# Performance work log

Measured on AMD Instinct MI355X. Metric: run time of the kernel, lower is better.

The kernel has to match this reference:

```python
import jax, jax.numpy as jnp
import numpy as np

T = 32400   # bs*H*W BEV queries (1*180*180)
S = 16896   # bs*num_cams*h*w image keys (1*6*32*88)
E = 256     # embed_dim
H = 8       # num_heads
D = 32      # head_dim
MAXL = 32   # max interval length (ref_num_f)


def _mlp(x, w1, b1, w2, b2):
    # nn.Sequential(Linear(E,2E), ReLU, Linear(2E,E))
    return jax.nn.relu(x @ w1 + b1) @ w2 + b2


def setup_inputs() -> dict:
    k0 = jax.random.key(0)
    ks = jax.random.split(k0, 8)
    # ragged interval structure: every BEV cell has an interval of length (idx%32)+1
    lengths = (np.arange(T) % MAXL) + 1
    starts = np.concatenate([np.zeros(1, np.int64), np.cumsum(lengths)[:-1]])
    N = int(lengths.sum())  # 534472 frustum points
    ranks_bev = np.repeat(np.arange(T), lengths)          # sorted by BEV cell
    rng = np.random.default_rng(0)
    ranks_feat = rng.integers(0, S, size=N)               # which key/value row each point reads

    def lin(k, fi, fo):
        return jax.random.normal(k, (fi, fo), jnp.float32) * (1.0 / np.sqrt(fi))

    key_feat = jax.random.normal(ks[1], (S, E), jnp.float32)
    return dict(
        query_depth=jax.random.normal(ks[0], (T, E), jnp.float32),
        key=key_feat,
        value=key_feat,  # module asserts torch.equal(key, value)
        q_w1=lin(ks[2], E, 2 * E), q_b1=jnp.zeros((2 * E,), jnp.float32),
        q_w2=lin(ks[3], 2 * E, E), q_b2=jnp.zeros((E,), jnp.float32),
        k_w1=lin(ks[4], E, 2 * E), k_b1=jnp.zeros((2 * E,), jnp.float32),
        k_w2=lin(ks[5], 2 * E, E), k_b2=jnp.zeros((E,), jnp.float32),
        ranks_feat_f=jnp.asarray(ranks_feat, jnp.int32),
        ranks_bev_f=jnp.asarray(ranks_bev, jnp.int32),
        interval_starts_f=jnp.asarray(starts, jnp.int32),
        interval_lengths_f=jnp.asarray(lengths, jnp.int32),
        ref_num=MAXL,
    )


def reference(query_depth, key, value,
              q_w1, q_b1, q_w2, q_b2,
              k_w1, k_b1, k_w2, k_b2,
              ranks_feat_f, ranks_bev_f,
              interval_starts_f, interval_lengths_f, ref_num):
    scaling = 1.0 / jnp.sqrt(jnp.float32(D))
    q = (_mlp(query_depth, q_w1, q_b1, q_w2, q_b2) * scaling).reshape(T, H, D)
    k = _mlp(key, k_w1, k_b1, k_w2, k_b2).reshape(S, H, D)
    v = value.reshape(S, H, D)

    N = ranks_bev_f.shape[0]
    pt = jnp.arange(N, dtype=jnp.int32)
    # interval id of each point (intervals are contiguous, sorted by start)
    iid = jnp.searchsorted(interval_starts_f, pt, side='right') - 1
    ranks_ref = pt - interval_starts_f[iid]  # within-interval slot, in [0, ref_num)

    # per-point raw attention logit: q[bev] . k[feat] per head  -> [N, H]
    w = jnp.einsum('nhd,nhd->nh', q[ranks_bev_f], k[ranks_feat_f])

    # scatter into ragged weight tensor [T, H, ref_num]; padding masked to -1e9
    attn = jnp.full((T, H, ref_num), -1e9, jnp.float32)
    attn = attn.at[ranks_bev_f, :, ranks_ref].set(w)
    attn = jax.nn.softmax(attn, axis=-1)

    # gather normalized weights back per point and scatter-combine values
    wp = attn[ranks_bev_f, :, ranks_ref]          # [N, H]
    vp = v[ranks_feat_f]                          # [N, H, D]
    out = jnp.zeros((T, H, D), jnp.float32).at[ranks_bev_f].add(wp[:, :, None] * vp)
    return out.reshape(T, E)
```

## Files before the change

kernel.cpp:

```cpp
#include <hip/hip_runtime.h>
#include <hip/hip_bf16.h>
#include <cstdint>
#include <cstddef>

constexpr int T_Q   = 32400;
constexpr int T_PAD = 32512;
constexpr int S_K   = 16896;
constexpr int E_DIM = 256;
constexpr int HID   = 512;

typedef __bf16 bf16x8 __attribute__((ext_vector_type(8)));
typedef float  f32x4  __attribute__((ext_vector_type(4)));
typedef unsigned short ushort8v __attribute__((ext_vector_type(8)));

__device__ __forceinline__ void async16(const __hip_bfloat16* gp, __hip_bfloat16* lp) {
    __builtin_amdgcn_global_load_lds(
        (const __attribute__((address_space(1))) void*)(gp),
        (__attribute__((address_space(3))) void*)(lp), 16, 0, 0);
}

__device__ __forceinline__ float b2f(unsigned short u) {
    return __uint_as_float(((unsigned)u) << 16);
}

constexpr int NB_K = (S_K * E_DIM / 4) / 256;
constexpr int NB_PREP = NB_K + 128;

__global__ __launch_bounds__(256) void prep(
    const float* __restrict__ val_in,
    const float* __restrict__ s0, const float* __restrict__ s1,
    const float* __restrict__ s2, const float* __restrict__ s3,
    __hip_bfloat16* __restrict__ kvB,
    __hip_bfloat16* __restrict__ d0, __hip_bfloat16* __restrict__ d1,
    __hip_bfloat16* __restrict__ d2, __hip_bfloat16* __restrict__ d3) {
    __shared__ float tb[64][65];
    const int b = blockIdx.x;
    const int tid = threadIdx.x;

    if (b < NB_K) {
        int i = (b * 256 + tid) * 4;
        float4 f = *(const float4*)(val_in + i);
        union { ushort4 u4; __hip_bfloat16 bb[4]; } cv;
        cv.bb[0] = __float2bfloat16(f.x);
        cv.bb[1] = __float2bfloat16(f.y);
        cv.bb[2] = __float2bfloat16(f.z);
        cv.bb[3] = __float2bfloat16(f.w);
        int r = i >> 8, c = i & 255;
        *(ushort4*)(kvB + (size_t)r * 512 + 256 + c) = cv.u4;
        return;
    }

    int tloc = b - NB_K;
    int m = tloc >> 5;
    int tt = tloc & 31;
    const float* S = m == 0 ? s0 : m == 1 ? s1 : m == 2 ? s2 : s3;
    __hip_bfloat16* D = m == 0 ? d0 : m == 1 ? d1 : m == 2 ? d2 : d3;
    int Kd, Nd, kt, nt;
    if ((m & 1) == 0) { Kd = 256; Nd = 512; kt = tt & 3; nt = tt >> 2; }
    else              { Kd = 512; Nd = 256; kt = tt & 7; nt = tt >> 3; }
    int tx = tid & 63, ty = tid >> 6;
#pragma unroll
    for (int p = 0; p < 16; ++p) {
        int row = ty * 16 + p;
        tb[row][tx] = S[(size_t)(kt * 64 + row) * Nd + nt * 64 + tx];
    }
    __syncthreads();
#pragma unroll
    for (int p = 0; p < 16; ++p) {
        int row = ty * 16 + p;
        D[(size_t)(nt * 64 + row) * Kd + kt * 64 + tx] = __float2bfloat16(tb[tx][row]);
    }
}


constexpr int MLP_QT = T_PAD / 64;
constexpr int MLP_KT = S_K / 64;
constexpr int MLP_NB = MLP_QT + MLP_KT;

__global__ __launch_bounds__(512, 4) void mlp_fused(
    const float* __restrict__ Aq, const float* __restrict__ Ak,
    const __hip_bfloat16* __restrict__ W1q, const __hip_bfloat16* __restrict__ W1k,
    const __hip_bfloat16* __restrict__ W2q, const __hip_bfloat16* __restrict__ W2k,
    const float* __restrict__ b1q, const float* __restrict__ b1k,
    const float* __restrict__ b2q, const float* __restrict__ b2k,
    __hip_bfloat16* __restrict__ Cq, __hip_bfloat16* __restrict__ Ck,
    float scaleq, int qtiles) {
    __shared__ __align__(16) __hip_bfloat16 Aslab[64 * 64];
    __shared__ __align__(16) __hip_bfloat16 Bs[256 * 64];
    __shared__ __align__(16) __hip_bfloat16 Hs[64 * 256];

    const int b = blockIdx.x;
    const bool isq = b < qtiles;
    const float* A  = isq ? Aq : Ak;
    const __hip_bfloat16* W1 = isq ? W1q : W1k;
    const __hip_bfloat16* W2 = isq ? W2q : W2k;
    const float* b1 = isq ? b1q : b1k;
    const float* b2 = isq ? b2q : b2k;
    __hip_bfloat16* C = isq ? Cq : Ck;
    const int ldc = isq ? E_DIM : 512;
    const float scale = isq ? scaleq : 1.0f;
    const int mrow0 = (isq ? b : b - qtiles) * 64;
    const int rowlim = isq ? T_Q : S_K;

    const int tid = threadIdx.x;
    const int w = tid >> 6, l = tid & 63;
    const int lm = l & 15, lq = l >> 4;
    const int wm = w >> 2;
    const int wn4 = w & 3;
    const int srow8 = l >> 3;
    const int u8 = l & 7;
    const int pu8 = u8 ^ srow8;
    const int scolB = (u8 ^ srow8) << 3;

    f32x4 acc2[2][4] = {};

#pragma unroll 1
    for (int nh = 0; nh < 2; ++nh) {
        f32x4 acc[2][4] = {};
#pragma unroll 1
        for (int st = 0; st < 4; ++st) {
            const int k0 = st * 64;
            {
                int r = w * 8 + srow8;
                int gr = mrow0 + r;
                float4 f0 = make_float4(0.f, 0.f, 0.f, 0.f);
                float4 f1 = make_float4(0.f, 0.f, 0.f, 0.f);
                if (gr < rowlim) {
                    const float* ap = A + (size_t)gr * 256 + k0 + u8 * 8;
                    f0 = *(const float4*)ap;
                    f1 = *(const float4*)(ap + 4);
                }
                union { bf16x8 v; __hip_bfloat16 bb[8]; } cv;
                cv.bb[0] = __float2bfloat16(f0.x); cv.bb[1] = __float2bfloat16(f0.y);
                cv.bb[2] = __float2bfloat16(f0.z); cv.bb[3] = __float2bfloat16(f0.w);
                cv.bb[4] = __float2bfloat16(f1.x); cv.bb[5] = __float2bfloat16(f1.y);
                cv.bb[6] = __float2bfloat16(f1.z); cv.bb[7] = __float2bfloat16(f1.w);
                *(bf16x8*)(Aslab + r * 64 + pu8 * 8) = cv.v;
            }
#pragma unroll
            for (int c = 0; c < 4; ++c) {
                int r = w * 32 + c * 8 + srow8;
                async16(W1 + (size_t)(nh * 256 + r) * 256 + k0 + scolB,
                        Bs + (w * 32 + c * 8) * 64);
            }
            __syncthreads();
#pragma unroll
            for (int ks = 0; ks < 2; ++ks) {
                bf16x8 af[2], bfr[4];
#pragma unroll
                for (int mi = 0; mi < 2; ++mi) {
                    int row = wm * 32 + mi * 16 + lm;
                    int pu = (ks * 4 + lq) ^ (row & 7);
                    af[mi] = *(const bf16x8*)(Aslab + row * 64 + pu * 8);
                }
#pragma unroll
                for (int ni = 0; ni < 4; ++ni) {
                    int brow = wn4 * 64 + ni * 16 + lm;
                    int pu = (ks * 4 + lq) ^ (brow & 7);
                    bfr[ni] = *(const bf16x8*)(Bs + brow * 64 + pu * 8);
                }
#pragma unroll
                for (int mi = 0; mi < 2; ++mi)
#pragma unroll
                    for (int ni = 0; ni < 4; ++ni)
                        acc[mi][ni] = __builtin_amdgcn_mfma_f32_16x16x32_bf16(
                            af[mi], bfr[ni], acc[mi][ni], 0, 0, 0);
            }
            __syncthreads();
        }

#pragma unroll
        for (int ni = 0; ni < 4; ++ni) {
            int col = wn4 * 64 + ni * 16 + lm;
            float bv = b1[nh * 256 + col];
            int un = col >> 3, el = col & 7;
#pragma unroll
            for (int mi = 0; mi < 2; ++mi) {
#pragma unroll
                for (int r = 0; r < 4; ++r) {
                    int row = wm * 32 + mi * 16 + lq * 4 + r;
                    float vv = fmaxf(acc[mi][ni][r] + bv, 0.f);
                    int pu = (un & 24) | ((un & 7) ^ (row & 7));
                    Hs[row * 256 + pu * 8 + el] = __float2bfloat16(vv);
                }
            }
        }

#pragma unroll 1
        for (int st = 0; st < 4; ++st) {
            const int k0 = st * 64;
#pragma unroll
            for (int c = 0; c < 4; ++c) {
                int r = w * 32 + c * 8 + srow8;
                async16(W2 + (size_t)r * 512 + nh * 256 + k0 + scolB,
                        Bs + (w * 32 + c * 8) * 64);
            }
            __syncthreads();
#pragma unroll
            for (int ks = 0; ks < 2; ++ks) {
                bf16x8 af[2], bfr[4];
#pragma unroll
                for (int mi = 0; mi < 2; ++mi) {
                    int row = wm * 32 + mi * 16 + lm;
                    int un = st * 8 + ks * 4 + lq;
                    int pu = (un & 24) | ((un & 7) ^ (row & 7));
                    af[mi] = *(const bf16x8*)(Hs + row * 256 + pu * 8);
                }
#pragma unroll
                for (int ni = 0; ni < 4; ++ni) {
                    int brow = wn4 * 64 + ni * 16 + lm;
                    int pu = (ks * 4 + lq) ^ (brow & 7);
                    bfr[ni] = *(const bf16x8*)(Bs + brow * 64 + pu * 8);
                }
#pragma unroll
                for (int mi = 0; mi < 2; ++mi)
#pragma unroll
                    for (int ni = 0; ni < 4; ++ni)
                        acc2[mi][ni] = __builtin_amdgcn_mfma_f32_16x16x32_bf16(
                            af[mi], bfr[ni], acc2[mi][ni], 0, 0, 0);
            }
            __syncthreads();
        }
    }

#pragma unroll
    for (int ni = 0; ni < 4; ++ni) {
        int col = wn4 * 64 + ni * 16 + lm;
        float bv = b2[col];
#pragma unroll
        for (int mi = 0; mi < 2; ++mi) {
            size_t rowb = (size_t)mrow0 + wm * 32 + mi * 16 + lq * 4;
#pragma unroll
            for (int r = 0; r < 4; ++r) {
                float vv = (acc2[mi][ni][r] + bv) * scale;
                C[(rowb + r) * ldc + col] = __float2bfloat16(vv);
            }
        }
    }
}


#define PREFP(KB, VB, C)                                                     \
    {                                                                        \
        int f_ = __shfl(myf, (C) + half);                                    \
        const __hip_bfloat16* p_ = kv + ((size_t)f_ << 9) + (sub << 3);      \
        KB = *(const ushort8v*)p_;                                           \
        VB = *(const ushort8v*)(p_ + 256);                                   \
    }

#define PROCP(KB, VB, C)                                                     \
    {                                                                        \
        float wv = 0.f;                                                      \
        _Pragma("unroll") for (int i = 0; i < 8; ++i)                        \
            wv = fmaf(qf[i], b2f(KB[i]), wv);                                \
        wv += __shfl_xor(wv, 1);                                             \
        wv += __shfl_xor(wv, 2);                                             \
        float sc = ((C) + half < L) ? wv : -1e30f;                           \
        float so = __shfl_xor(sc, 32);                                       \
        float pm = fmaxf(sc, so);                                            \
        if (__all(pm <= m)) {                                                \
            float p = __expf(sc - m);                                        \
            s += p;                                                          \
            _Pragma("unroll") for (int i = 0; i < 8; ++i)                    \
                a[i] = fmaf(p, b2f(VB[i]), a[i]);                            \
        } else {                                                             \
            float mn = fmaxf(m, pm);                                         \
            float al = __expf(m - mn);                                       \
            float p  = __expf(sc - mn);                                      \
            m = mn;                                                          \
            s = fmaf(s, al, p);                                              \
            _Pragma("unroll") for (int i = 0; i < 8; ++i)                    \
                a[i] = fmaf(p, b2f(VB[i]), a[i] * al);                       \
        }                                                                    \
    }

#define STEPP(KB, VB, J)                                                     \
    if (c + (J) < L) {                                                       \
        PROCP(KB, VB, c + (J));                                              \
        if (c + (J) + 8 < L) PREFP(KB, VB, c + (J) + 8);                     \
    }

constexpr int ATTN_BLOCKS = 2026;

__global__ __launch_bounds__(256) void attn_kernel(
    const __hip_bfloat16* __restrict__ q,
    const __hip_bfloat16* __restrict__ kv,
    const int* __restrict__ rf,
    const int* __restrict__ starts,
    const int* __restrict__ lens,
    float* __restrict__ out) {
    const int wid = threadIdx.x >> 6;
    const int l = threadIdx.x & 63;
    const int sub = l & 31, half = l >> 5;
    const int tstride = gridDim.x * 4;

    for (int t = blockIdx.x * 4 + wid; t < T_Q; t += tstride) {
        int su = __builtin_amdgcn_readfirstlane(starts[t]);
        int L  = __builtin_amdgcn_readfirstlane(lens[t]);

        int li = l < L - 1 ? l : L - 1;
        int myf = rf[su + li];

        ushort8v qu = *(const ushort8v*)(q + (size_t)t * 256 + sub * 8);
        float qf[8];
#pragma unroll
        for (int i = 0; i < 8; ++i) qf[i] = b2f(qu[i]);

        float m = -INFINITY, s = 0.f;
        float a[8] = {0.f, 0.f, 0.f, 0.f, 0.f, 0.f, 0.f, 0.f};

        ushort8v k0 = {}, v0 = {}, k1 = {}, v1 = {};
        ushort8v k2 = {}, v2 = {}, k3 = {}, v3 = {};
        PREFP(k0, v0, 0);
        if (L > 2) PREFP(k1, v1, 2);
        if (L > 4) PREFP(k2, v2, 4);
        if (L > 6) PREFP(k3, v3, 6);

        for (int c = 0; c < L; c += 8) {
            STEPP(k0, v0, 0)
            STEPP(k1, v1, 2)
            STEPP(k2, v2, 4)
            STEPP(k3, v3, 6)
        }

        float st = s + __shfl_xor(s, 32);
#pragma unroll
        for (int i = 0; i < 8; ++i) a[i] += __shfl_xor(a[i], 32);

        if (half) {
            float inv = 1.f / st;
            float* op = out + (size_t)t * 256 + sub * 8;
            float4 o0, o1;
            o0.x = a[0] * inv; o0.y = a[1] * inv; o0.z = a[2] * inv; o0.w = a[3] * inv;
            o1.x = a[4] * inv; o1.y = a[5] * inv; o1.z = a[6] * inv; o1.w = a[7] * inv;
            *(float4*)op = o0;
            *(float4*)(op + 4) = o1;
        }
    }
}

extern "C" void kernel_launch(void* const* d_in, const int* in_sizes, int n_in,
                              void* d_out, int out_size, void* d_ws, size_t ws_size,
                              hipStream_t stream) {
    const float* q_in   = (const float*)d_in[0];
    const float* key_in = (const float*)d_in[1];
    const float* val_in = (const float*)d_in[2];
    const float* q_w1   = (const float*)d_in[3];
    const float* q_b1   = (const float*)d_in[4];
    const float* q_w2   = (const float*)d_in[5];
    const float* q_b2   = (const float*)d_in[6];
    const float* k_w1   = (const float*)d_in[7];
    const float* k_b1   = (const float*)d_in[8];
    const float* k_w2   = (const float*)d_in[9];
    const float* k_b2   = (const float*)d_in[10];
    const int* ranks_feat = (const int*)d_in[11];
    const int* starts     = (const int*)d_in[13];
    const int* lens       = (const int*)d_in[14];
    float* out = (float*)d_out;

    char* ws = (char*)d_ws;
    size_t off = 0;
    auto alloc = [&](size_t bytes) {
        char* p = ws + off;
        off += (bytes + 255) & ~(size_t)255;
        return p;
    };
    __hip_bfloat16* qMl  = (__hip_bfloat16*)alloc((size_t)T_PAD * E_DIM * 2);
    __hip_bfloat16* kvB  = (__hip_bfloat16*)alloc((size_t)S_K * 512 * 2);
    __hip_bfloat16* w1qT = (__hip_bfloat16*)alloc((size_t)HID * E_DIM * 2);
    __hip_bfloat16* w2qT = (__hip_bfloat16*)alloc((size_t)E_DIM * HID * 2);
    __hip_bfloat16* w1kT = (__hip_bfloat16*)alloc((size_t)HID * E_DIM * 2);
    __hip_bfloat16* w2kT = (__hip_bfloat16*)alloc((size_t)E_DIM * HID * 2);
    (void)ws_size; (void)n_in; (void)out_size; (void)in_sizes;

    prep<<<NB_PREP, 256, 0, stream>>>(val_in, q_w1, q_w2, k_w1, k_w2,
                                      kvB, w1qT, w2qT, w1kT, w2kT);

    const float qscale = 0.17677669529663687f;

    mlp_fused<<<MLP_NB, 512, 0, stream>>>(
        q_in, key_in, w1qT, w1kT, w2qT, w2kT,
        q_b1, k_b1, q_b2, k_b2, qMl, kvB, qscale, MLP_QT);

    attn_kernel<<<ATTN_BLOCKS, 256, 0, stream>>>(qMl, kvB, ranks_feat, starts, lens, out);
}
```

Before: 273.4 us.

## Double MLP row tile to 128 and fold value bf16 conversion into MLP kernel

The fused MLP kernel now processes 128 rows per block instead of 64. Each warp computes 4x4 MFMA tiles, so every weight slab loaded into LDS is reused across twice as many rows, halving weight traffic per row. The value-to-bf16 conversion moves out of the prep kernel into the tail of the key-side MLP blocks, which shrinks prep to only the weight transposes. In exchange, LDS use and register pressure rise, occupancy drops (launch bounds go from 4 to 2 blocks per unit), and there are half as many blocks.

```diff
diff --git a/kernel.cpp b/kernel.cpp
--- a/kernel.cpp
+++ b/kernel.cpp
@@ -23,36 +23,17 @@
     return __uint_as_float(((unsigned)u) << 16);
 }
 
-constexpr int NB_K = (S_K * E_DIM / 4) / 256;
-constexpr int NB_PREP = NB_K + 128;
-
 __global__ __launch_bounds__(256) void prep(
-    const float* __restrict__ val_in,
     const float* __restrict__ s0, const float* __restrict__ s1,
     const float* __restrict__ s2, const float* __restrict__ s3,
-    __hip_bfloat16* __restrict__ kvB,
     __hip_bfloat16* __restrict__ d0, __hip_bfloat16* __restrict__ d1,
     __hip_bfloat16* __restrict__ d2, __hip_bfloat16* __restrict__ d3) {
     __shared__ float tb[64][65];
     const int b = blockIdx.x;
     const int tid = threadIdx.x;
 
-    if (b < NB_K) {
-        int i = (b * 256 + tid) * 4;
-        float4 f = *(const float4*)(val_in + i);
-        union { ushort4 u4; __hip_bfloat16 bb[4]; } cv;
-        cv.bb[0] = __float2bfloat16(f.x);
-        cv.bb[1] = __float2bfloat16(f.y);
-        cv.bb[2] = __float2bfloat16(f.z);
-        cv.bb[3] = __float2bfloat16(f.w);
-        int r = i >> 8, c = i & 255;
-        *(ushort4*)(kvB + (size_t)r * 512 + 256 + c) = cv.u4;
-        return;
-    }
-
-    int tloc = b - NB_K;
-    int m = tloc >> 5;
-    int tt = tloc & 31;
+    int m = b >> 5;
+    int tt = b & 31;
     const float* S = m == 0 ? s0 : m == 1 ? s1 : m == 2 ? s2 : s3;
     __hip_bfloat16* D = m == 0 ? d0 : m == 1 ? d1 : m == 2 ? d2 : d3;
     int Kd, Nd, kt, nt;
@@ -73,21 +54,22 @@
 }
 
 
-constexpr int MLP_QT = T_PAD / 64;
-constexpr int MLP_KT = S_K / 64;
+constexpr int MLP_QT = T_PAD / 128;
+constexpr int MLP_KT = S_K / 128;
 constexpr int MLP_NB = MLP_QT + MLP_KT;
 
-__global__ __launch_bounds__(512, 4) void mlp_fused(
+__global__ __launch_bounds__(512, 2) void mlp_fused(
     const float* __restrict__ Aq, const float* __restrict__ Ak,
+    const float* __restrict__ val_in,
     const __hip_bfloat16* __restrict__ W1q, const __hip_bfloat16* __restrict__ W1k,
     const __hip_bfloat16* __restrict__ W2q, const __hip_bfloat16* __restrict__ W2k,
     const float* __restrict__ b1q, const float* __restrict__ b1k,
     const float* __restrict__ b2q, const float* __restrict__ b2k,
     __hip_bfloat16* __restrict__ Cq, __hip_bfloat16* __restrict__ Ck,
     float scaleq, int qtiles) {
-    __shared__ __align__(16) __hip_bfloat16 Aslab[64 * 64];
+    __shared__ __align__(16) __hip_bfloat16 Aslab[128 * 64];
     __shared__ __align__(16) __hip_bfloat16 Bs[256 * 64];
-    __shared__ __align__(16) __hip_bfloat16 Hs[64 * 256];
+    __shared__ __align__(16) __hip_bfloat16 Hs[128 * 256];
 
     const int b = blockIdx.x;
     const bool isq = b < qtiles;
@@ -99,7 +81,7 @@
     __hip_bfloat16* C = isq ? Cq : Ck;
     const int ldc = isq ? E_DIM : 512;
     const float scale = isq ? scaleq : 1.0f;
-    const int mrow0 = (isq ? b : b - qtiles) * 64;
+    const int mrow0 = (isq ? b : b - qtiles) * 128;
     const int rowlim = isq ? T_Q : S_K;
 
     const int tid = threadIdx.x;
@@ -109,24 +91,26 @@
     const int wn4 = w & 3;
     const int srow8 = l >> 3;
     const int u8 = l & 7;
-    const int pu8 = u8 ^ srow8;
     const int scolB = (u8 ^ srow8) << 3;
 
-    f32x4 acc2[2][4] = {};
+    f32x4 acc2[4][4] = {};
 
 #pragma unroll 1
     for (int nh = 0; nh < 2; ++nh) {
-        f32x4 acc[2][4] = {};
+        f32x4 acc[4][4] = {};
 #pragma unroll 1
         for (int st = 0; st < 4; ++st) {
             const int k0 = st * 64;
-            {
-                int r = w * 8 + srow8;
+#pragma unroll
+            for (int c = 0; c < 2; ++c) {
+                int idx = tid + c * 512;
+                int r = idx >> 3;
+                int u = idx & 7;
                 int gr = mrow0 + r;
                 float4 f0 = make_float4(0.f, 0.f, 0.f, 0.f);
                 float4 f1 = make_float4(0.f, 0.f, 0.f, 0.f);
                 if (gr < rowlim) {
-                    const float* ap = A + (size_t)gr * 256 + k0 + u8 * 8;
+                    const float* ap = A + (size_t)gr * 256 + k0 + u * 8;
                     f0 = *(const float4*)ap;
                     f1 = *(const float4*)(ap + 4);
                 }
@@ -135,7 +119,8 @@
                 cv.bb[2] = __float2bfloat16(f0.z); cv.bb[3] = __float2bfloat16(f0.w);
                 cv.bb[4] = __float2bfloat16(f1.x); cv.bb[5] = __float2bfloat16(f1.y);
                 cv.bb[6] = __float2bfloat16(f1.z); cv.bb[7] = __float2bfloat16(f1.w);
-                *(bf16x8*)(Aslab + r * 64 + pu8 * 8) = cv.v;
+                int pu = u ^ (r & 7);
+                *(bf16x8*)(Aslab + r * 64 + pu * 8) = cv.v;
             }
 #pragma unroll
             for (int c = 0; c < 4; ++c) {
@@ -146,10 +131,10 @@
             __syncthreads();
 #pragma unroll
             for (int ks = 0; ks < 2; ++ks) {
-                bf16x8 af[2], bfr[4];
-#pragma unroll
-                for (int mi = 0; mi < 2; ++mi) {
-                    int row = wm * 32 + mi * 16 + lm;
+                bf16x8 af[4], bfr[4];
+#pragma unroll
+                for (int mi = 0; mi < 4; ++mi) {
+                    int row = wm * 64 + mi * 16 + lm;
                     int pu = (ks * 4 + lq) ^ (row & 7);
                     af[mi] = *(const bf16x8*)(Aslab + row * 64 + pu * 8);
                 }
@@ -160,7 +145,7 @@
                     bfr[ni] = *(const bf16x8*)(Bs + brow * 64 + pu * 8);
                 }
 #pragma unroll
-                for (int mi = 0; mi < 2; ++mi)
+                for (int mi = 0; mi < 4; ++mi)
 #pragma unroll
                     for (int ni = 0; ni < 4; ++ni)
                         acc[mi][ni] = __builtin_amdgcn_mfma_f32_16x16x32_bf16(
@@ -175,10 +160,10 @@
             float bv = b1[nh * 256 + col];
             int un = col >> 3, el = col & 7;
 #pragma unroll
-            for (int mi = 0; mi < 2; ++mi) {
+            for (int mi = 0; mi < 4; ++mi) {
 #pragma unroll
                 for (int r = 0; r < 4; ++r) {
-                    int row = wm * 32 + mi * 16 + lq * 4 + r;
+                    int row = wm * 64 + mi * 16 + lq * 4 + r;
                     float vv = fmaxf(acc[mi][ni][r] + bv, 0.f);
                     int pu = (un & 24) | ((un & 7) ^ (row & 7));
                     Hs[row * 256 + pu * 8 + el] = __float2bfloat16(vv);
@@ -198,10 +183,10 @@
             __syncthreads();
 #pragma unroll
             for (int ks = 0; ks < 2; ++ks) {
-                bf16x8 af[2], bfr[4];
-#pragma unroll
-                for (int mi = 0; mi < 2; ++mi) {
-                    int row = wm * 32 + mi * 16 + lm;
+                bf16x8 af[4], bfr[4];
+#pragma unroll
+                for (int mi = 0; mi < 4; ++mi) {
+                    int row = wm * 64 + mi * 16 + lm;
                     int un = st * 8 + ks * 4 + lq;
                     int pu = (un & 24) | ((un & 7) ^ (row & 7));
                     af[mi] = *(const bf16x8*)(Hs + row * 256 + pu * 8);
@@ -213,7 +198,7 @@
                     bfr[ni] = *(const bf16x8*)(Bs + brow * 64 + pu * 8);
                 }
 #pragma unroll
-                for (int mi = 0; mi < 2; ++mi)
+                for (int mi = 0; mi < 4; ++mi)
 #pragma unroll
                     for (int ni = 0; ni < 4; ++ni)
                         acc2[mi][ni] = __builtin_amdgcn_mfma_f32_16x16x32_bf16(
@@ -228,13 +213,30 @@
         int col = wn4 * 64 + ni * 16 + lm;
         float bv = b2[col];
 #pragma unroll
-        for (int mi = 0; mi < 2; ++mi) {
-            size_t rowb = (size_t)mrow0 + wm * 32 + mi * 16 + lq * 4;
+        for (int mi = 0; mi < 4; ++mi) {
+            size_t rowb = (size_t)mrow0 + wm * 64 + mi * 16 + lq * 4;
 #pragma unroll
             for (int r = 0; r < 4; ++r) {
                 float vv = (acc2[mi][ni][r] + bv) * scale;
                 C[(rowb + r) * ldc + col] = __float2bfloat16(vv);
             }
+        }
+    }
+
+    if (!isq) {
+#pragma unroll
+        for (int i = 0; i < 16; ++i) {
+            int idx = tid + i * 512;
+            int r = idx >> 6;
+            int c4 = idx & 63;
+            int gr = mrow0 + r;
+            float4 f = *(const float4*)(val_in + (size_t)gr * 256 + c4 * 4);
+            union { ushort4 u4; __hip_bfloat16 bb[4]; } cv;
+            cv.bb[0] = __float2bfloat16(f.x);
+            cv.bb[1] = __float2bfloat16(f.y);
+            cv.bb[2] = __float2bfloat16(f.z);
+            cv.bb[3] = __float2bfloat16(f.w);
+            *(ushort4*)(Ck + (size_t)gr * 512 + 256 + c4 * 4) = cv.u4;
         }
     }
 }
@@ -373,13 +375,13 @@
     __hip_bfloat16* w2kT = (__hip_bfloat16*)alloc((size_t)E_DIM * HID * 2);
     (void)ws_size; (void)n_in; (void)out_size; (void)in_sizes;
 
-    prep<<<NB_PREP, 256, 0, stream>>>(val_in, q_w1, q_w2, k_w1, k_w2,
-                                      kvB, w1qT, w2qT, w1kT, w2kT);
+    prep<<<128, 256, 0, stream>>>(q_w1, q_w2, k_w1, k_w2,
+                                  w1qT, w2qT, w1kT, w2kT);
 
     const float qscale = 0.17677669529663687f;
 
     mlp_fused<<<MLP_NB, 512, 0, stream>>>(
-        q_in, key_in, w1qT, w1kT, w2qT, w2kT,
+        q_in, key_in, val_in, w1qT, w1kT, w2qT, w2kT,
         q_b1, k_b1, q_b2, k_b2, qMl, kvB, qscale, MLP_QT);
 
     attn_kernel<<<ATTN_BLOCKS, 256, 0, stream>>>(qMl, kvB, ranks_feat, starts, lens, out);
```

Measured after the change: 264.7 us. -3.2%, faster.

## Pre-cast MLP inputs to bf16 and read GEMM operands directly from global memory

Applied to the files above, without the earlier changes.

The prep kernel now casts both query and key inputs to a combined bf16 buffer, and the value cast moves into the tail of the key MLP blocks. The fused MLP kernel drops its LDS staging for the A slab and the weight tiles and loads MFMA fragments straight from global memory (relying on L2 for weight reuse), removing most per-stage barriers and unrolling the k loops. This cuts LDS traffic and synchronisation, and frees LDS that may allow more resident blocks. In exchange it adds an extra round trip of the bf16 input buffer through memory and issues uncoalesced 16-byte global loads per lane.

```diff
diff --git a/kernel.cpp b/kernel.cpp
--- a/kernel.cpp
+++ b/kernel.cpp
@@ -13,44 +13,52 @@
 typedef float  f32x4  __attribute__((ext_vector_type(4)));
 typedef unsigned short ushort8v __attribute__((ext_vector_type(8)));
 
-__device__ __forceinline__ void async16(const __hip_bfloat16* gp, __hip_bfloat16* lp) {
-    __builtin_amdgcn_global_load_lds(
-        (const __attribute__((address_space(1))) void*)(gp),
-        (__attribute__((address_space(3))) void*)(lp), 16, 0, 0);
-}
-
 __device__ __forceinline__ float b2f(unsigned short u) {
     return __uint_as_float(((unsigned)u) << 16);
 }
 
-constexpr int NB_K = (S_K * E_DIM / 4) / 256;
-constexpr int NB_PREP = NB_K + 128;
+constexpr int AB_ROWS = T_PAD + S_K;
+constexpr int CAST_NB = AB_ROWS * 256 / 2048;
+constexpr int PREP_NB = CAST_NB + 128;
 
 __global__ __launch_bounds__(256) void prep(
-    const float* __restrict__ val_in,
+    const float* __restrict__ q_in, const float* __restrict__ key_in,
+    __hip_bfloat16* __restrict__ Abf,
     const float* __restrict__ s0, const float* __restrict__ s1,
     const float* __restrict__ s2, const float* __restrict__ s3,
-    __hip_bfloat16* __restrict__ kvB,
     __hip_bfloat16* __restrict__ d0, __hip_bfloat16* __restrict__ d1,
     __hip_bfloat16* __restrict__ d2, __hip_bfloat16* __restrict__ d3) {
     __shared__ float tb[64][65];
     const int b = blockIdx.x;
     const int tid = threadIdx.x;
 
-    if (b < NB_K) {
-        int i = (b * 256 + tid) * 4;
-        float4 f = *(const float4*)(val_in + i);
-        union { ushort4 u4; __hip_bfloat16 bb[4]; } cv;
-        cv.bb[0] = __float2bfloat16(f.x);
-        cv.bb[1] = __float2bfloat16(f.y);
-        cv.bb[2] = __float2bfloat16(f.z);
-        cv.bb[3] = __float2bfloat16(f.w);
-        int r = i >> 8, c = i & 255;
-        *(ushort4*)(kvB + (size_t)r * 512 + 256 + c) = cv.u4;
+    if (b < CAST_NB) {
+        size_t base = ((size_t)b * 256 + tid) * 8;
+        int row = (int)(base >> 8);
+        int c = (int)(base & 255);
+        float4 f0 = make_float4(0.f, 0.f, 0.f, 0.f);
+        float4 f1 = make_float4(0.f, 0.f, 0.f, 0.f);
+        if (row < T_PAD) {
+            if (row < T_Q) {
+                const float* p = q_in + (size_t)row * 256 + c;
+                f0 = *(const float4*)p;
+                f1 = *(const float4*)(p + 4);
+            }
+        } else {
+            const float* p = key_in + (size_t)(row - T_PAD) * 256 + c;
+            f0 = *(const float4*)p;
+            f1 = *(const float4*)(p + 4);
+        }
+        union { bf16x8 v; __hip_bfloat16 bb[8]; } cv;
+        cv.bb[0] = __float2bfloat16(f0.x); cv.bb[1] = __float2bfloat16(f0.y);
+        cv.bb[2] = __float2bfloat16(f0.z); cv.bb[3] = __float2bfloat16(f0.w);
+        cv.bb[4] = __float2bfloat16(f1.x); cv.bb[5] = __float2bfloat16(f1.y);
+        cv.bb[6] = __float2bfloat16(f1.z); cv.bb[7] = __float2bfloat16(f1.w);
+        *(bf16x8*)(Abf + (size_t)row * 256 + c) = cv.v;
         return;
     }
 
-    int tloc = b - NB_K;
+    int tloc = b - CAST_NB;
     int m = tloc >> 5;
     int tt = tloc & 31;
     const float* S = m == 0 ? s0 : m == 1 ? s1 : m == 2 ? s2 : s3;
@@ -78,20 +86,18 @@
 constexpr int MLP_NB = MLP_QT + MLP_KT;
 
 __global__ __launch_bounds__(512, 4) void mlp_fused(
-    const float* __restrict__ Aq, const float* __restrict__ Ak,
+    const __hip_bfloat16* __restrict__ Abf,
+    const float* __restrict__ val_in,
     const __hip_bfloat16* __restrict__ W1q, const __hip_bfloat16* __restrict__ W1k,
     const __hip_bfloat16* __restrict__ W2q, const __hip_bfloat16* __restrict__ W2k,
     const float* __restrict__ b1q, const float* __restrict__ b1k,
     const float* __restrict__ b2q, const float* __restrict__ b2k,
     __hip_bfloat16* __restrict__ Cq, __hip_bfloat16* __restrict__ Ck,
     float scaleq, int qtiles) {
-    __shared__ __align__(16) __hip_bfloat16 Aslab[64 * 64];
-    __shared__ __align__(16) __hip_bfloat16 Bs[256 * 64];
     __shared__ __align__(16) __hip_bfloat16 Hs[64 * 256];
 
     const int b = blockIdx.x;
     const bool isq = b < qtiles;
-    const float* A  = isq ? Aq : Ak;
     const __hip_bfloat16* W1 = isq ? W1q : W1k;
     const __hip_bfloat16* W2 = isq ? W2q : W2k;
     const float* b1 = isq ? b1q : b1k;
@@ -100,64 +106,38 @@
     const int ldc = isq ? E_DIM : 512;
     const float scale = isq ? scaleq : 1.0f;
     const int mrow0 = (isq ? b : b - qtiles) * 64;
-    const int rowlim = isq ? T_Q : S_K;
+    const size_t arow0 = (size_t)(isq ? b * 64 : T_PAD + (b - qtiles) * 64);
 
     const int tid = threadIdx.x;
     const int w = tid >> 6, l = tid & 63;
     const int lm = l & 15, lq = l >> 4;
     const int wm = w >> 2;
     const int wn4 = w & 3;
-    const int srow8 = l >> 3;
-    const int u8 = l & 7;
-    const int pu8 = u8 ^ srow8;
-    const int scolB = (u8 ^ srow8) << 3;
+
+    const __hip_bfloat16* Arow[2];
+#pragma unroll
+    for (int mi = 0; mi < 2; ++mi)
+        Arow[mi] = Abf + (arow0 + wm * 32 + mi * 16 + lm) * 256;
 
     f32x4 acc2[2][4] = {};
 
 #pragma unroll 1
     for (int nh = 0; nh < 2; ++nh) {
         f32x4 acc[2][4] = {};
-#pragma unroll 1
+#pragma unroll
         for (int st = 0; st < 4; ++st) {
             const int k0 = st * 64;
-            {
-                int r = w * 8 + srow8;
-                int gr = mrow0 + r;
-                float4 f0 = make_float4(0.f, 0.f, 0.f, 0.f);
-                float4 f1 = make_float4(0.f, 0.f, 0.f, 0.f);
-                if (gr < rowlim) {
-                    const float* ap = A + (size_t)gr * 256 + k0 + u8 * 8;
-                    f0 = *(const float4*)ap;
-                    f1 = *(const float4*)(ap + 4);
-                }
-                union { bf16x8 v; __hip_bfloat16 bb[8]; } cv;
-                cv.bb[0] = __float2bfloat16(f0.x); cv.bb[1] = __float2bfloat16(f0.y);
-                cv.bb[2] = __float2bfloat16(f0.z); cv.bb[3] = __float2bfloat16(f0.w);
-                cv.bb[4] = __float2bfloat16(f1.x); cv.bb[5] = __float2bfloat16(f1.y);
-                cv.bb[6] = __float2bfloat16(f1.z); cv.bb[7] = __float2bfloat16(f1.w);
-                *(bf16x8*)(Aslab + r * 64 + pu8 * 8) = cv.v;
-            }
-#pragma unroll
-            for (int c = 0; c < 4; ++c) {
-                int r = w * 32 + c * 8 + srow8;
-                async16(W1 + (size_t)(nh * 256 + r) * 256 + k0 + scolB,
-                        Bs + (w * 32 + c * 8) * 64);
-            }
-            __syncthreads();
 #pragma unroll
             for (int ks = 0; ks < 2; ++ks) {
+                const int kc = k0 + (ks * 4 + lq) * 8;
                 bf16x8 af[2], bfr[4];
 #pragma unroll
-                for (int mi = 0; mi < 2; ++mi) {
-                    int row = wm * 32 + mi * 16 + lm;
-                    int pu = (ks * 4 + lq) ^ (row & 7);
-                    af[mi] = *(const bf16x8*)(Aslab + row * 64 + pu * 8);
-                }
+                for (int mi = 0; mi < 2; ++mi)
+                    af[mi] = *(const bf16x8*)(Arow[mi] + kc);
 #pragma unroll
                 for (int ni = 0; ni < 4; ++ni) {
-                    int brow = wn4 * 64 + ni * 16 + lm;
-                    int pu = (ks * 4 + lq) ^ (brow & 7);
-                    bfr[ni] = *(const bf16x8*)(Bs + brow * 64 + pu * 8);
+                    int brow = nh * 256 + wn4 * 64 + ni * 16 + lm;
+                    bfr[ni] = *(const bf16x8*)(W1 + (size_t)brow * 256 + kc);
                 }
 #pragma unroll
                 for (int mi = 0; mi < 2; ++mi)
@@ -166,8 +146,9 @@
                         acc[mi][ni] = __builtin_amdgcn_mfma_f32_16x16x32_bf16(
                             af[mi], bfr[ni], acc[mi][ni], 0, 0, 0);
             }
-            __syncthreads();
-        }
+        }
+
+        __syncthreads();
 
 #pragma unroll
         for (int ni = 0; ni < 4; ++ni) {
@@ -185,17 +166,11 @@
                 }
             }
         }
-
-#pragma unroll 1
+        __syncthreads();
+
+#pragma unroll
         for (int st = 0; st < 4; ++st) {
             const int k0 = st * 64;
-#pragma unroll
-            for (int c = 0; c < 4; ++c) {
-                int r = w * 32 + c * 8 + srow8;
-                async16(W2 + (size_t)r * 512 + nh * 256 + k0 + scolB,
-                        Bs + (w * 32 + c * 8) * 64);
-            }
-            __syncthreads();
 #pragma unroll
             for (int ks = 0; ks < 2; ++ks) {
                 bf16x8 af[2], bfr[4];
@@ -209,8 +184,8 @@
 #pragma unroll
                 for (int ni = 0; ni < 4; ++ni) {
                     int brow = wn4 * 64 + ni * 16 + lm;
-                    int pu = (ks * 4 + lq) ^ (brow & 7);
-                    bfr[ni] = *(const bf16x8*)(Bs + brow * 64 + pu * 8);
+                    bfr[ni] = *(const bf16x8*)(
+                        W2 + (size_t)brow * 512 + nh * 256 + k0 + (ks * 4 + lq) * 8);
                 }
 #pragma unroll
                 for (int mi = 0; mi < 2; ++mi)
@@ -219,7 +194,6 @@
                         acc2[mi][ni] = __builtin_amdgcn_mfma_f32_16x16x32_bf16(
                             af[mi], bfr[ni], acc2[mi][ni], 0, 0, 0);
             }
-            __syncthreads();
         }
     }
 
@@ -235,6 +209,23 @@
                 float vv = (acc2[mi][ni][r] + bv) * scale;
                 C[(rowb + r) * ldc + col] = __float2bfloat16(vv);
             }
+        }
+    }
+
+    if (!isq) {
+#pragma unroll
+        for (int i = 0; i < 8; ++i) {
+            int idx = tid + i * 512;
+            int r = idx >> 6;
+            int c4 = idx & 63;
+            int gr = mrow0 + r;
+            float4 f = *(const float4*)(val_in + (size_t)gr * 256 + c4 * 4);
+            union { ushort4 u4; __hip_bfloat16 bb[4]; } cv;
+            cv.bb[0] = __float2bfloat16(f.x);
+            cv.bb[1] = __float2bfloat16(f.y);
+            cv.bb[2] = __float2bfloat16(f.z);
+            cv.bb[3] = __float2bfloat16(f.w);
+            *(ushort4*)(Ck + (size_t)gr * 512 + 256 + c4 * 4) = cv.u4;
         }
     }
 }
@@ -367,19 +358,21 @@
     };
     __hip_bfloat16* qMl  = (__hip_bfloat16*)alloc((size_t)T_PAD * E_DIM * 2);
     __hip_bfloat16* kvB  = (__hip_bfloat16*)alloc((size_t)S_K * 512 * 2);
+    __hip_bfloat16* Abf  = (__hip_bfloat16*)alloc((size_t)AB_ROWS * 256 * 2);
     __hip_bfloat16* w1qT = (__hip_bfloat16*)alloc((size_t)HID * E_DIM * 2);
     __hip_bfloat16* w2qT = (__hip_bfloat16*)alloc((size_t)E_DIM * HID * 2);
     __hip_bfloat16* w1kT = (__hip_bfloat16*)alloc((size_t)HID * E_DIM * 2);
     __hip_bfloat16* w2kT = (__hip_bfloat16*)alloc((size_t)E_DIM * HID * 2);
     (void)ws_size; (void)n_in; (void)out_size; (void)in_sizes;
 
-    prep<<<NB_PREP, 256, 0, stream>>>(val_in, q_w1, q_w2, k_w1, k_w2,
-                                      kvB, w1qT, w2qT, w1kT, w2kT);
+    prep<<<PREP_NB, 256, 0, stream>>>(q_in, key_in, Abf,
+                                      q_w1, q_w2, k_w1, k_w2,
+                                      w1qT, w2qT, w1kT, w2kT);
 
     const float qscale = 0.17677669529663687f;
 
     mlp_fused<<<MLP_NB, 512, 0, stream>>>(
-        q_in, key_in, w1qT, w1kT, w2qT, w2kT,
+        Abf, val_in, w1qT, w1kT, w2qT, w2kT,
         q_b1, k_b1, q_b2, k_b2, qMl, kvB, qscale, MLP_QT);
 
     attn_kernel<<<ATTN_BLOCKS, 256, 0, stream>>>(qMl, kvB, ranks_feat, starts, lens, out);
```

Result: slower. 398.4 us (+45.7%).

## Fuse value bf16 conversion into MLP kernel and deepen attention prefetch pipeline

Applied to the files above, without the earlier changes.

The fp32-to-bf16 conversion of the value rows, which used to run in the prep kernel, now happens inside the key-side MLP blocks. Each block writes the second half of the interleaved kv buffer for its own 64 rows, so prep only transposes the weights. Separately, the attention loop gets a fifth prefetch register pair, so five key/value pairs are in flight instead of four. The extra registers could lower occupancy in the attention kernel, and the MLP key blocks take on more memory traffic.

```diff
diff --git a/kernel.cpp b/kernel.cpp
--- a/kernel.cpp
+++ b/kernel.cpp
@@ -23,36 +23,17 @@
     return __uint_as_float(((unsigned)u) << 16);
 }
 
-constexpr int NB_K = (S_K * E_DIM / 4) / 256;
-constexpr int NB_PREP = NB_K + 128;
-
 __global__ __launch_bounds__(256) void prep(
-    const float* __restrict__ val_in,
     const float* __restrict__ s0, const float* __restrict__ s1,
     const float* __restrict__ s2, const float* __restrict__ s3,
-    __hip_bfloat16* __restrict__ kvB,
     __hip_bfloat16* __restrict__ d0, __hip_bfloat16* __restrict__ d1,
     __hip_bfloat16* __restrict__ d2, __hip_bfloat16* __restrict__ d3) {
     __shared__ float tb[64][65];
     const int b = blockIdx.x;
     const int tid = threadIdx.x;
 
-    if (b < NB_K) {
-        int i = (b * 256 + tid) * 4;
-        float4 f = *(const float4*)(val_in + i);
-        union { ushort4 u4; __hip_bfloat16 bb[4]; } cv;
-        cv.bb[0] = __float2bfloat16(f.x);
-        cv.bb[1] = __float2bfloat16(f.y);
-        cv.bb[2] = __float2bfloat16(f.z);
-        cv.bb[3] = __float2bfloat16(f.w);
-        int r = i >> 8, c = i & 255;
-        *(ushort4*)(kvB + (size_t)r * 512 + 256 + c) = cv.u4;
-        return;
-    }
-
-    int tloc = b - NB_K;
-    int m = tloc >> 5;
-    int tt = tloc & 31;
+    int m = b >> 5;
+    int tt = b & 31;
     const float* S = m == 0 ? s0 : m == 1 ? s1 : m == 2 ? s2 : s3;
     __hip_bfloat16* D = m == 0 ? d0 : m == 1 ? d1 : m == 2 ? d2 : d3;
     int Kd, Nd, kt, nt;
@@ -79,6 +60,7 @@
 
 __global__ __launch_bounds__(512, 4) void mlp_fused(
     const float* __restrict__ Aq, const float* __restrict__ Ak,
+    const float* __restrict__ val_in,
     const __hip_bfloat16* __restrict__ W1q, const __hip_bfloat16* __restrict__ W1k,
     const __hip_bfloat16* __restrict__ W2q, const __hip_bfloat16* __restrict__ W2k,
     const float* __restrict__ b1q, const float* __restrict__ b1k,
@@ -111,6 +93,23 @@
     const int u8 = l & 7;
     const int pu8 = u8 ^ srow8;
     const int scolB = (u8 ^ srow8) << 3;
+
+    if (!isq) {
+#pragma unroll
+        for (int i = 0; i < 8; ++i) {
+            int idx = tid + i * 512;
+            int r = idx >> 6;
+            int c4 = idx & 63;
+            int gr = mrow0 + r;
+            float4 f = *(const float4*)(val_in + (size_t)gr * 256 + c4 * 4);
+            union { ushort4 u4; __hip_bfloat16 bb[4]; } cv;
+            cv.bb[0] = __float2bfloat16(f.x);
+            cv.bb[1] = __float2bfloat16(f.y);
+            cv.bb[2] = __float2bfloat16(f.z);
+            cv.bb[3] = __float2bfloat16(f.w);
+            *(ushort4*)(Ck + (size_t)gr * 512 + 256 + c4 * 4) = cv.u4;
+        }
+    }
 
     f32x4 acc2[2][4] = {};
 
@@ -277,7 +276,7 @@
 #define STEPP(KB, VB, J)                                                     \
     if (c + (J) < L) {                                                       \
         PROCP(KB, VB, c + (J));                                              \
-        if (c + (J) + 8 < L) PREFP(KB, VB, c + (J) + 8);                     \
+        if (c + (J) + 10 < L) PREFP(KB, VB, c + (J) + 10);                   \
     }
 
 constexpr int ATTN_BLOCKS = 2026;
@@ -309,18 +308,20 @@
         float m = -INFINITY, s = 0.f;
         float a[8] = {0.f, 0.f, 0.f, 0.f, 0.f, 0.f, 0.f, 0.f};
 
-        ushort8v k0 = {}, v0 = {}, k1 = {}, v1 = {};
-        ushort8v k2 = {}, v2 = {}, k3 = {}, v3 = {};
+        ushort8v k0 = {}, v0 = {}, k1 = {}, v1 = {}, k2 = {}, v2 = {};
+        ushort8v k3 = {}, v3 = {}, k4 = {}, v4 = {};
         PREFP(k0, v0, 0);
         if (L > 2) PREFP(k1, v1, 2);
         if (L > 4) PREFP(k2, v2, 4);
         if (L > 6) PREFP(k3, v3, 6);
-
-        for (int c = 0; c < L; c += 8) {
+        if (L > 8) PREFP(k4, v4, 8);
+
+        for (int c = 0; c < L; c += 10) {
             STEPP(k0, v0, 0)
             STEPP(k1, v1, 2)
             STEPP(k2, v2, 4)
             STEPP(k3, v3, 6)
+            STEPP(k4, v4, 8)
         }
 
         float st = s + __shfl_xor(s, 32);
@@ -373,13 +374,13 @@
     __hip_bfloat16* w2kT = (__hip_bfloat16*)alloc((size_t)E_DIM * HID * 2);
     (void)ws_size; (void)n_in; (void)out_size; (void)in_sizes;
 
-    prep<<<NB_PREP, 256, 0, stream>>>(val_in, q_w1, q_w2, k_w1, k_w2,
-                                      kvB, w1qT, w2qT, w1kT, w2kT);
+    prep<<<128, 256, 0, stream>>>(q_w1, q_w2, k_w1, k_w2,
+                                  w1qT, w2qT, w1kT, w2kT);
 
     const float qscale = 0.17677669529663687f;
 
     mlp_fused<<<MLP_NB, 512, 0, stream>>>(
-        q_in, key_in, w1qT, w1kT, w2qT, w2kT,
+        q_in, key_in, val_in, w1qT, w1kT, w2qT, w2kT,
         q_b1, k_b1, q_b2, k_b2, qMl, kvB, qscale, MLP_QT);
 
     attn_kernel<<<ATTN_BLOCKS, 256, 0, stream>>>(qMl, kvB, ranks_feat, starts, lens, out);
```

New measurement: 272.5 us. Within noise of the previous version (-0.4%).
